# Kernel tuning notes

Hardware: AMD Instinct MI355X
Metric: run time of the kernel (lower is better)

Reference implementation:

```python
import jax, jax.numpy as jnp
import numpy as np

D_VOCAB, D_MODEL, N_CTX, D_MLP, D_HEAD, N_HEADS, N_LAYERS = 32000, 1024, 2048, 4096, 64, 16, 4
BATCH, SEQ = 2, 2048


def setup_inputs() -> dict:
    key = jax.random.key(0)
    ks = jax.random.split(key, 12)
    sd = 1.0 / np.sqrt(D_MODEL)
    inp = {
        'tokens': jax.random.randint(ks[0], (BATCH, SEQ), 0, D_VOCAB),
        'W_E': jax.random.normal(ks[1], (D_MODEL, D_VOCAB), jnp.float32) * sd,
        'W_pos': jax.random.normal(ks[2], (N_CTX, D_MODEL), jnp.float32) * sd,
        'W_K': jax.random.normal(ks[3], (N_LAYERS, N_HEADS, D_HEAD, D_MODEL), jnp.float32) * sd,
        'W_Q': jax.random.normal(ks[4], (N_LAYERS, N_HEADS, D_HEAD, D_MODEL), jnp.float32) * sd,
        'W_V': jax.random.normal(ks[5], (N_LAYERS, N_HEADS, D_HEAD, D_MODEL), jnp.float32) * sd,
        'W_O': jax.random.normal(ks[6], (N_LAYERS, D_MODEL, D_HEAD * N_HEADS), jnp.float32) * sd,
        'W_in': jax.random.normal(ks[7], (N_LAYERS, D_MLP, D_MODEL), jnp.float32) * sd,
        'b_in': jnp.zeros((N_LAYERS, D_MLP), jnp.float32),
        'W_out': jax.random.normal(ks[8], (N_LAYERS, D_MODEL, D_MLP), jnp.float32) * sd,
        'b_out': jnp.zeros((N_LAYERS, D_MODEL), jnp.float32),
        'W_U': jax.random.normal(ks[9], (D_MODEL, D_VOCAB), jnp.float32) / np.sqrt(D_VOCAB),
    }
    return inp


def reference(tokens, W_E, W_pos, W_K, W_Q, W_V, W_O, W_in, b_in, W_out, b_out, W_U):
    P = tokens.shape[-1]
    # Embed: einsum('dbp->bpd', W_E[:, x])  ==  W_E.T[tokens]
    x = W_E.T[tokens]                      # [b, p, d]
    x = x + W_pos[:P]                      # PosEmbed
    causal = jnp.tril(jnp.ones((P, P), dtype=bool))  # mask[q, p]: p <= q
    scale = 1.0 / np.sqrt(D_HEAD)
    for l in range(N_LAYERS):
        # --- Attention ---
        k = jnp.einsum('ihd,bpd->biph', W_K[l], x)
        q = jnp.einsum('ihd,bpd->biph', W_Q[l], x)
        v = jnp.einsum('ihd,bpd->biph', W_V[l], x)
        scores = jnp.einsum('biph,biqh->biqp', k, q)
        # tril(scores) - 1e10*(1-mask)  ==  where(mask, scores, -1e10)
        masked = jnp.where(causal, scores, jnp.float32(-1e10))
        attn = jax.nn.softmax(masked * scale, axis=-1)   # softmax over keys p
        z = jnp.einsum('biph,biqp->biqh', v, attn)       # [b, i, q, h]
        z_flat = jnp.transpose(z, (0, 2, 1, 3)).reshape(z.shape[0], P, -1)  # b q (i h)
        attn_out = jnp.einsum('df,bqf->bqd', W_O[l], z_flat)
        x = x + attn_out
        # --- MLP (ReLU) ---
        pre = jnp.einsum('md,bpd->bpm', W_in[l], x) + b_in[l]
        post = jax.nn.relu(pre)
        x = x + jnp.einsum('dm,bpm->bpd', W_out[l], post) + b_out[l]
    return x @ W_U                          # logits [b, p, d_vocab]
```

## Files before the change

### kernel.cpp

```cpp
#include <hip/hip_runtime.h>
#include <hip/hip_bf16.h>
#include <math.h>

#define DV   32000
#define DM   1024
#define DMLP 4096
#define DH   64
#define NH   16
#define NL   4
#define BATCH 2
#define S    2048
#define MTOK (BATCH*S)

typedef __bf16 bf16_t;
typedef bf16_t bf16x8 __attribute__((ext_vector_type(8)));
typedef float  f32x4  __attribute__((ext_vector_type(4)));

#define AS1 __attribute__((address_space(1)))
#define AS3 __attribute__((address_space(3)))

__device__ __forceinline__ void gload16(const bf16_t* g, bf16_t* l) {
    __builtin_amdgcn_global_load_lds((const AS1 void*)g, (AS3 void*)l, 16, 0, 0);
}

__device__ __forceinline__ unsigned short bfbits(float v) {
    union { bf16_t b; unsigned short u; } c; c.b = (bf16_t)v; return c.u;
}
__device__ __forceinline__ float b2f(unsigned short u) {
    union { float f; unsigned v; } c; c.v = ((unsigned)u) << 16; return c.f;
}

template<int MODE, bool BIAS, bool RELU>
__global__ __launch_bounds__(512, 1)
void gemm256(const bf16_t* __restrict__ A, const bf16_t* __restrict__ Bm,
             char* __restrict__ Out, int ldc,
             const float* __restrict__ bias, int K)
{
    const int mb = blockIdx.x, nb = blockIdx.y;

    __shared__ alignas(16) bf16_t lds[2][2][2][128*64];

    const int tid  = threadIdx.x;
    const int wave = tid >> 6, lane = tid & 63;
    const int wm = wave >> 2, wn = wave & 3;
    const int l16 = lane & 15, lh = lane >> 4;

    const bf16_t* Abase = A  + (long)(mb*256)*K;
    const bf16_t* Bbase = Bm + (long)(nb*256)*K;

    const int c0 = tid,       r0 = c0 >> 3, lc0 = (c0 & 7) ^ (r0 & 7);
    const int c1 = 512 + tid, r1 = c1 >> 3, lc1 = (c1 & 7) ^ (r1 & 7);

    auto stage = [&](int buf, int mat, int half, int k0) {
        const bf16_t* src = (mat ? Bbase : Abase) + (long)(half*128)*K + k0;
        bf16_t* dst = &lds[buf][mat][half][0];
        gload16(&src[(long)r0*K + lc0*8], dst + c0*8);
        gload16(&src[(long)r1*K + lc1*8], dst + c1*8);
    };

    f32x4 acc[8][4];
#pragma unroll
    for (int i=0;i<8;i++)
#pragma unroll
        for (int j=0;j<4;j++) { f32x4 zv={0.f,0.f,0.f,0.f}; acc[i][j]=zv; }

    const int NT = K >> 6;
    stage(0,0,0,0); stage(0,0,1,0); stage(0,1,0,0); stage(0,1,1,0);

    int cur = 0;
    for (int kt = 0; kt < NT; ++kt) {
        const int nxt = cur ^ 1;
        const int k1 = (kt+1) << 6;
        const bool more = (kt+1 < NT);

        if (more) {
            stage(nxt,0,0,k1);
            asm volatile("s_waitcnt vmcnt(2)" ::: "memory");
        } else {
            asm volatile("s_waitcnt vmcnt(0)" ::: "memory");
        }
        asm volatile("s_barrier" ::: "memory");

        bf16x8 af[4][2], bfr[4][2];
#pragma unroll
        for (int i=0;i<4;i++) {
            int ra = i*16 + l16;
#pragma unroll
            for (int kk=0;kk<2;kk++)
                af[i][kk] = *(const bf16x8*)&lds[cur][0][wm][ra*64 + (((kk*4+lh)^(ra&7))*8)];
        }
#pragma unroll
        for (int j=0;j<2;j++) {
            int rb = (wn&1)*64 + j*16 + l16;
#pragma unroll
            for (int kk=0;kk<2;kk++)
                bfr[j][kk] = *(const bf16x8*)&lds[cur][1][wn>>1][rb*64 + (((kk*4+lh)^(rb&7))*8)];
        }
        __builtin_amdgcn_s_setprio(1);
#pragma unroll
        for (int kk=0;kk<2;kk++)
#pragma unroll
            for (int i=0;i<4;i++)
#pragma unroll
                for (int j=0;j<2;j++)
                    acc[i][j] = __builtin_amdgcn_mfma_f32_16x16x32_bf16(af[i][kk], bfr[j][kk], acc[i][j], 0,0,0);
        __builtin_amdgcn_s_setprio(0);

        if (more) stage(nxt,0,1,k1);
#pragma unroll
        for (int j=2;j<4;j++) {
            int rb = (wn&1)*64 + j*16 + l16;
#pragma unroll
            for (int kk=0;kk<2;kk++)
                bfr[j][kk] = *(const bf16x8*)&lds[cur][1][wn>>1][rb*64 + (((kk*4+lh)^(rb&7))*8)];
        }
        __builtin_amdgcn_s_setprio(1);
#pragma unroll
        for (int kk=0;kk<2;kk++)
#pragma unroll
            for (int i=0;i<4;i++)
#pragma unroll
                for (int j=2;j<4;j++)
                    acc[i][j] = __builtin_amdgcn_mfma_f32_16x16x32_bf16(af[i][kk], bfr[j][kk], acc[i][j], 0,0,0);
        __builtin_amdgcn_s_setprio(0);

        if (more) stage(nxt,1,0,k1);
#pragma unroll
        for (int i=0;i<4;i++) {
            int ra = (i+4)*16 + l16;
#pragma unroll
            for (int kk=0;kk<2;kk++)
                af[i][kk] = *(const bf16x8*)&lds[cur][0][wm][ra*64 + (((kk*4+lh)^(ra&7))*8)];
        }
        __builtin_amdgcn_s_setprio(1);
#pragma unroll
        for (int kk=0;kk<2;kk++)
#pragma unroll
            for (int i=0;i<4;i++)
#pragma unroll
                for (int j=0;j<2;j++)
                    acc[i+4][j] = __builtin_amdgcn_mfma_f32_16x16x32_bf16(af[i][kk], bfr[j][kk], acc[i+4][j], 0,0,0);
        __builtin_amdgcn_s_setprio(0);

        if (more) stage(nxt,1,1,k1);
        __builtin_amdgcn_s_setprio(1);
#pragma unroll
        for (int kk=0;kk<2;kk++)
#pragma unroll
            for (int i=0;i<4;i++)
#pragma unroll
                for (int j=2;j<4;j++)
                    acc[i+4][j] = __builtin_amdgcn_mfma_f32_16x16x32_bf16(af[i][kk], bfr[j][kk], acc[i+4][j], 0,0,0);
        __builtin_amdgcn_s_setprio(0);

        asm volatile("s_barrier" ::: "memory");
        cur = nxt;
    }

    if constexpr (MODE == 1) {
        float* lsl = reinterpret_cast<float*>(&lds[0][0][0][0]) + wave*(32*68);
        const int lrow = lane >> 4;
        const int lcq  = lane & 15;
#pragma unroll
        for (int ch=0; ch<4; ++ch) {
#pragma unroll
            for (int il=0; il<2; ++il)
#pragma unroll
                for (int j=0;j<4;j++)
#pragma unroll
                    for (int r=0;r<4;r++)
                        lsl[(il*16 + lh*4 + r)*68 + j*16 + l16] = acc[ch*2+il][j][r];
#pragma unroll
            for (int u=0; u<8; ++u) {
                int rl = u*4 + lrow;
                f32x4 v = *(const f32x4*)&lsl[rl*68 + lcq*4];
                long row = mb*256 + wm*128 + ch*32 + rl;
                long col = nb*256 + wn*64 + lcq*4;
                __builtin_nontemporal_store(v, (f32x4*)&((float*)Out)[row*ldc + col]);
            }
        }
    } else {
#pragma unroll
        for (int i=0;i<8;i++) {
            int row0 = mb*256 + wm*128 + i*16 + lh*4;
#pragma unroll
            for (int j=0;j<4;j++) {
                int col = nb*256 + wn*64 + j*16 + l16;
                float bv = BIAS ? bias[col] : 0.0f;
#pragma unroll
                for (int r=0;r<4;r++) {
                    int row = row0 + r;
                    float v = acc[i][j][r] + bv;
                    if (RELU) v = v > 0.f ? v : 0.f;
                    ((bf16_t*)Out)[(long)row*ldc + col] = (bf16_t)v;
                }
            }
        }
    }
}

template<int BM, int BN, int MODE, bool BIAS, bool RELU>
__global__ __launch_bounds__(256)
void gemm_tn(const bf16_t* __restrict__ A, long sA,
             const bf16_t* __restrict__ Bm, long sB,
             char* __restrict__ Out, long sC, int ldc,
             const float* __restrict__ bias,
             float* __restrict__ resid, bf16_t* __restrict__ residb,
             int K)
{
    constexpr int BK = 64;
    constexpr int WM = BM/2, WN = BN/2;
    constexpr int FM = WM/16, FN = WN/16;
    constexpr int APASS = (BM*BK)/(256*8);
    constexpr int BPASS = (BN*BK)/(256*8);

    const int mb = blockIdx.x, nb = blockIdx.y;

    __shared__ alignas(16) bf16_t As[BM*BK];
    __shared__ alignas(16) bf16_t Bs[BN*BK];

    const int tid  = threadIdx.x;
    const int wave = tid >> 6, lane = tid & 63;
    const int wm = wave >> 1, wn = wave & 1;
    const int l16 = lane & 15, lh = lane >> 4;
    const long z = blockIdx.z;

    const bf16_t* Ab = A  + z*sA + (long)mb*BM*K;
    const bf16_t* Bb = Bm + z*sB + (long)nb*BN*K;

    f32x4 acc[FM][FN];
#pragma unroll
    for (int i=0;i<FM;i++)
#pragma unroll
        for (int j=0;j<FN;j++) { f32x4 zv = {0.f,0.f,0.f,0.f}; acc[i][j] = zv; }

    for (int k0 = 0; k0 < K; k0 += BK) {
        __syncthreads();
#pragma unroll
        for (int u=0; u<APASS; ++u) {
            int c = u*256 + tid;
            int row = c >> 3, lc = (c & 7) ^ (row & 7);
            gload16(&Ab[(long)row*K + k0 + lc*8], &As[c*8]);
        }
#pragma unroll
        for (int u=0; u<BPASS; ++u) {
            int c = u*256 + tid;
            int row = c >> 3, lc = (c & 7) ^ (row & 7);
            gload16(&Bb[(long)row*K + k0 + lc*8], &Bs[c*8]);
        }
        __syncthreads();

        bf16x8 af[FM][2], bfr[FN][2];
#pragma unroll
        for (int kk=0;kk<2;kk++) {
#pragma unroll
            for (int i=0;i<FM;i++) {
                int row = wm*WM + i*16 + l16;
                int pw = (kk*4 + lh) ^ (row & 7);
                af[i][kk] = *(const bf16x8*)&As[row*BK + pw*8];
            }
#pragma unroll
            for (int j=0;j<FN;j++) {
                int row = wn*WN + j*16 + l16;
                int pw = (kk*4 + lh) ^ (row & 7);
                bfr[j][kk] = *(const bf16x8*)&Bs[row*BK + pw*8];
            }
        }
#pragma unroll
        for (int kk=0;kk<2;kk++)
#pragma unroll
            for (int i=0;i<FM;i++)
#pragma unroll
                for (int j=0;j<FN;j++)
                    acc[i][j] = __builtin_amdgcn_mfma_f32_16x16x32_bf16(af[i][kk], bfr[j][kk], acc[i][j], 0,0,0);
    }

#pragma unroll
    for (int i=0;i<FM;i++) {
        int row0 = mb*BM + wm*WM + i*16 + lh*4;
#pragma unroll
        for (int j=0;j<FN;j++) {
            int col = nb*BN + wn*WN + j*16 + l16;
            float bv = BIAS ? bias[col] : 0.0f;
#pragma unroll
            for (int r=0;r<4;r++) {
                int row = row0 + r;
                float v = acc[i][j][r] + bv;
                if (RELU) v = v > 0.f ? v : 0.f;
                if constexpr (MODE == 0) {
                    long off = z*sC + (long)row*ldc + col;
                    ((bf16_t*)Out)[off] = (bf16_t)v;
                } else if constexpr (MODE == 1) {
                    long off = z*sC + (long)row*ldc + col;
                    ((float*)Out)[off] = v;
                } else {
                    long o2 = (long)row*ldc + col;
                    float nv = resid[o2] + v;
                    resid[o2]  = nv;
                    residb[o2] = (bf16_t)nv;
                }
            }
        }
    }
}

__global__ __launch_bounds__(256)
void flash_attn(const bf16_t* __restrict__ qkvf,
                const bf16_t* __restrict__ vtg,
                bf16_t* __restrict__ zf)
{
    const int qt = blockIdx.x;
    const int bh = blockIdx.y;
    const int b  = bh >> 4, hd = bh & 15;

    __shared__ alignas(16) bf16_t Kl[64*64];
    __shared__ alignas(16) bf16_t Vtl[64*64];
    __shared__ alignas(16) bf16_t Pl[4*32*64];

    const int tid = threadIdx.x;
    const int wave = tid >> 6, lane = tid & 63;
    const int l16 = lane & 15, lh = lane >> 4;
    const int wq_lo = qt*128 + wave*32;
    bf16_t* Pw = Pl + wave*32*64;

    bf16x8 qr[2][2];
#pragma unroll
    for (int qf=0; qf<2; qf++) {
        int qg = wq_lo + qf*16 + l16;
#pragma unroll
        for (int dhh=0; dhh<2; dhh++)
            qr[qf][dhh] = *(const bf16x8*)&qkvf[((long)b*S + qg)*3072 + hd*64 + dhh*32 + lh*8];
    }

    f32x4 o[4][2];
#pragma unroll
    for (int d=0; d<4; d++)
#pragma unroll
        for (int qf=0; qf<2; qf++) { f32x4 zv={0.f,0.f,0.f,0.f}; o[d][qf]=zv; }
    float mrun[2] = {-1e30f, -1e30f};
    float lrun[2] = {0.f, 0.f};

    const int nt = 2*(qt+1);
    const float C = 0.125f;

    for (int t = 0; t < nt; ++t) {
        const int kv0 = t*64;
        __syncthreads();
#pragma unroll
        for (int u=0; u<2; ++u) {
            int c = u*256 + tid;
            int row = c >> 3, lc = (c & 7) ^ (row & 7);
            gload16(&qkvf[((long)b*S + kv0 + row)*3072 + 1024 + hd*64 + lc*8], &Kl[c*8]);
        }
#pragma unroll
        for (int u=0; u<2; ++u) {
            int c = u*256 + tid;
            int row = c >> 3, lc = (c & 7) ^ (row & 7);
            gload16(&vtg[((long)bh*DH + row)*S + kv0 + lc*8], &Vtl[c*8]);
        }
        __syncthreads();

        f32x4 s[4][2];
#pragma unroll
        for (int f=0; f<4; f++)
#pragma unroll
            for (int qf=0; qf<2; qf++) { f32x4 zv={0.f,0.f,0.f,0.f}; s[f][qf]=zv; }
        __builtin_amdgcn_s_setprio(1);
#pragma unroll
        for (int f=0; f<4; f++) {
            int krow = f*16 + l16;
#pragma unroll
            for (int dhh=0; dhh<2; dhh++) {
                bf16x8 kfr = *(const bf16x8*)&Kl[krow*64 + (((dhh*4+lh) ^ (krow&7))*8)];
#pragma unroll
                for (int qf=0; qf<2; qf++)
                    s[f][qf] = __builtin_amdgcn_mfma_f32_16x16x32_bf16(kfr, qr[qf][dhh], s[f][qf], 0,0,0);
            }
        }
        __builtin_amdgcn_s_setprio(0);

        const bool needmask = (kv0 + 64 > wq_lo);

#pragma unroll
        for (int qf=0; qf<2; qf++) {
            int qg = wq_lo + qf*16 + l16;
            float pmax = -1e30f;
#pragma unroll
            for (int f=0; f<4; f++)
#pragma unroll
                for (int r=0; r<4; r++) {
                    float sv = s[f][qf][r];
                    if (needmask && (kv0 + f*16 + lh*4 + r > qg)) { sv = -1e30f; s[f][qf][r] = sv; }
                    pmax = fmaxf(pmax, sv);
                }
            pmax = fmaxf(pmax, __shfl_xor(pmax, 16));
            pmax = fmaxf(pmax, __shfl_xor(pmax, 32));
            float mnew = fmaxf(mrun[qf], pmax);
            float corr = __expf((mrun[qf] - mnew)*C);
            mrun[qf] = mnew;
            lrun[qf] *= corr;
#pragma unroll
            for (int d=0; d<4; d++) o[d][qf] *= corr;
            float lsum = 0.f;
            int qloc = qf*16 + l16;
#pragma unroll
            for (int f=0; f<4; f++) {
                ushort4 pk;
                float p0 = __expf((s[f][qf][0]-mnew)*C);
                float p1 = __expf((s[f][qf][1]-mnew)*C);
                float p2 = __expf((s[f][qf][2]-mnew)*C);
                float p3 = __expf((s[f][qf][3]-mnew)*C);
                lsum += (p0+p1) + (p2+p3);
                pk.x = bfbits(p0); pk.y = bfbits(p1); pk.z = bfbits(p2); pk.w = bfbits(p3);
                int phys = (f*2 + (lh>>1)) ^ (qloc & 7);
                *(ushort4*)&Pw[qloc*64 + phys*8 + (lh&1)*4] = pk;
            }
            lrun[qf] += lsum;
        }

#pragma unroll
        for (int kh=0; kh<2; kh++) {
            bf16x8 pb[2];
#pragma unroll
            for (int qf=0; qf<2; qf++) {
                int qloc = qf*16 + l16;
                pb[qf] = *(const bf16x8*)&Pw[qloc*64 + (((kh*4+lh) ^ (qloc&7))*8)];
            }
            __builtin_amdgcn_s_setprio(1);
#pragma unroll
            for (int d=0; d<4; d++) {
                int vrow = d*16 + l16;
                bf16x8 va = *(const bf16x8*)&Vtl[vrow*64 + (((kh*4+lh) ^ (vrow&7))*8)];
#pragma unroll
                for (int qf=0; qf<2; qf++)
                    o[d][qf] = __builtin_amdgcn_mfma_f32_16x16x32_bf16(va, pb[qf], o[d][qf], 0,0,0);
            }
            __builtin_amdgcn_s_setprio(0);
        }
    }

#pragma unroll
    for (int qf=0; qf<2; qf++) {
        float lt = lrun[qf];
        lt += __shfl_xor(lt, 16);
        lt += __shfl_xor(lt, 32);
        float inv = 1.0f / lt;
        int qg = wq_lo + qf*16 + l16;
#pragma unroll
        for (int d=0; d<4; d++) {
            ushort4 ov;
            ov.x = bfbits(o[d][qf][0]*inv);
            ov.y = bfbits(o[d][qf][1]*inv);
            ov.z = bfbits(o[d][qf][2]*inv);
            ov.w = bfbits(o[d][qf][3]*inv);
            *(ushort4*)&zf[((long)b*S + qg)*DM + hd*64 + d*16 + lh*4] = ov;
        }
    }
}

__global__ __launch_bounds__(256) void k_conv_qkv(
    const float* __restrict__ Wq, const float* __restrict__ Wk,
    const float* __restrict__ Wv, bf16_t* __restrict__ out)
{
    long idx = (long)blockIdx.x*256 + threadIdx.x;
    long l = idx / (3072L*DM);
    long r = idx % (3072L*DM);
    int row = (int)(r / DM), d = (int)(r % DM);
    int sel = row >> 10, rr = row & 1023;
    const float* src = sel==0 ? Wq : (sel==1 ? Wk : Wv);
    out[idx] = (bf16_t)src[(l*1024 + rr)*(long)DM + d];
}

__global__ __launch_bounds__(256) void k_conv(const float* __restrict__ src,
                                              bf16_t* __restrict__ dst, long n)
{
    long i = ((long)blockIdx.x*256 + threadIdx.x)*4;
    if (i >= n) return;
    float4 v = *(const float4*)&src[i];
    dst[i+0]=(bf16_t)v.x; dst[i+1]=(bf16_t)v.y; dst[i+2]=(bf16_t)v.z; dst[i+3]=(bf16_t)v.w;
}

__global__ __launch_bounds__(256) void k_trans(const float* __restrict__ W,
                                               bf16_t* __restrict__ out, int NC)
{
    __shared__ float tile[32][33];
    int n0 = blockIdx.x*32, k0 = blockIdx.y*32;
    int tx = threadIdx.x & 31, ty = threadIdx.x >> 5;
#pragma unroll
    for (int u=0;u<4;u++)
        tile[ty+u*8][tx] = W[(long)(k0+ty+u*8)*NC + n0+tx];
    __syncthreads();
#pragma unroll
    for (int u=0;u<4;u++)
        out[(long)(n0+ty+u*8)*DM + k0+tx] = (bf16_t)tile[tx][ty+u*8];
}

__global__ __launch_bounds__(256) void k_embed(const int* __restrict__ tok,
    const bf16_t* __restrict__ WEt, const float* __restrict__ Wpos,
    float* __restrict__ xf, bf16_t* __restrict__ xb)
{
    int bp = blockIdx.x;
    int p  = bp & (S-1);
    int t  = tok[bp];
    int d  = threadIdx.x*4;
    ushort4 e = *(const ushort4*)&WEt[(long)t*DM + d];
    float4  w = *(const float4*)&Wpos[(long)p*DM + d];
    float4 v;
    v.x = b2f(e.x)+w.x; v.y = b2f(e.y)+w.y; v.z = b2f(e.z)+w.z; v.w = b2f(e.w)+w.w;
    *(float4*)&xf[(long)bp*DM + d] = v;
    ushort4 o;
    o.x = bfbits(v.x); o.y = bfbits(v.y); o.z = bfbits(v.z); o.w = bfbits(v.w);
    *(ushort4*)&xb[(long)bp*DM + d] = o;
}

__global__ __launch_bounds__(256) void k_permv(const bf16_t* __restrict__ qkv,
    bf16_t* __restrict__ vt)
{
    __shared__ bf16_t tile[64][66];
    const int p0 = blockIdx.x*64;
    const int bh = blockIdx.y;
    const int b  = bh >> 4, hd = bh & 15;
    const int tx = threadIdx.x & 63, ty = threadIdx.x >> 6;
#pragma unroll
    for (int u=0;u<16;u++) {
        int r = u*4 + ty;
        tile[r][tx] = qkv[((long)b*S + p0 + r)*3072 + 2048 + hd*64 + tx];
    }
    __syncthreads();
#pragma unroll
    for (int u=0;u<16;u++) {
        int hh = u*4 + ty;
        vt[(((long)bh)*DH + hh)*S + p0 + tx] = tile[tx][hh];
    }
}

extern "C" void kernel_launch(void* const* d_in, const int* in_sizes, int n_in,
                              void* d_out, int out_size, void* d_ws, size_t ws_size,
                              hipStream_t stream)
{
    const int*   tokens = (const int*)d_in[0];
    const float* W_E    = (const float*)d_in[1];
    const float* W_pos  = (const float*)d_in[2];
    const float* W_K    = (const float*)d_in[3];
    const float* W_Q    = (const float*)d_in[4];
    const float* W_V    = (const float*)d_in[5];
    const float* W_O    = (const float*)d_in[6];
    const float* W_in   = (const float*)d_in[7];
    const float* b_in   = (const float*)d_in[8];
    const float* W_out  = (const float*)d_in[9];
    const float* b_out  = (const float*)d_in[10];
    const float* W_U    = (const float*)d_in[11];
    float* out = (float*)d_out;

    char* ws = (char*)d_ws;
    long off = 0;
    auto alloc = [&](long bytes)->char* {
        char* p = ws + off; off += (bytes + 255) & ~255L; return p;
    };
    bf16_t* wqkv = (bf16_t*)alloc((long)NL*3072*DM*2);
    bf16_t* wo   = (bf16_t*)alloc((long)NL*DM*DM*2);
    bf16_t* win  = (bf16_t*)alloc((long)NL*DMLP*DM*2);
    bf16_t* wout = (bf16_t*)alloc((long)NL*DM*DMLP*2);
    bf16_t* wut  = (bf16_t*)alloc((long)DV*DM*2);
    bf16_t* wet  = (bf16_t*)alloc((long)DV*DM*2);
    float*  xf   = (float*)alloc((long)MTOK*DM*4);
    bf16_t* xb   = (bf16_t*)alloc((long)MTOK*DM*2);
    bf16_t* qkvf = (bf16_t*)alloc((long)MTOK*3072*2);
    bf16_t* vt   = (bf16_t*)alloc((long)BATCH*NH*S*DH*2);
    bf16_t* zf   = (bf16_t*)alloc((long)MTOK*DM*2);
    bf16_t* post = (bf16_t*)alloc((long)MTOK*DMLP*2);

    k_conv_qkv<<<(int)(((long)NL*3072*DM)/256), 256, 0, stream>>>(W_Q, W_K, W_V, wqkv);
    k_conv<<<(int)(((long)NL*DM*DM)/1024),   256, 0, stream>>>(W_O,   wo,   (long)NL*DM*DM);
    k_conv<<<(int)(((long)NL*DMLP*DM)/1024), 256, 0, stream>>>(W_in,  win,  (long)NL*DMLP*DM);
    k_conv<<<(int)(((long)NL*DM*DMLP)/1024), 256, 0, stream>>>(W_out, wout, (long)NL*DM*DMLP);
    k_trans<<<dim3(DV/32, DM/32), 256, 0, stream>>>(W_U, wut, DV);
    k_trans<<<dim3(DV/32, DM/32), 256, 0, stream>>>(W_E, wet, DV);

    k_embed<<<MTOK, 256, 0, stream>>>(tokens, wet, W_pos, xf, xb);

    for (int l = 0; l < NL; ++l) {
        gemm256<0,false,false><<<dim3(MTOK/256, 3072/256), 512, 0, stream>>>(
            xb, wqkv + (long)l*3072*DM, (char*)qkvf, 3072, nullptr, DM);
        k_permv<<<dim3(S/64, BATCH*NH), 256, 0, stream>>>(qkvf, vt);

        flash_attn<<<dim3(S/128, BATCH*NH), 256, 0, stream>>>(qkvf, vt, zf);

        gemm_tn<128,128,2,false,false><<<dim3(MTOK/128, DM/128, 1), 256, 0, stream>>>(
            zf, 0L, wo + (long)l*DM*DM, 0L, nullptr, 0L, DM,
            nullptr, xf, xb, DM);
        gemm256<0,true,true><<<dim3(MTOK/256, DMLP/256), 512, 0, stream>>>(
            xb, win + (long)l*DMLP*DM, (char*)post, DMLP,
            b_in + (long)l*DMLP, DM);
        gemm_tn<128,128,2,true,false><<<dim3(MTOK/128, DM/128, 1), 256, 0, stream>>>(
            post, 0L, wout + (long)l*DM*DMLP, 0L, nullptr, 0L, DM,
            b_out + (long)l*DM, xf, xb, DMLP);
    }

    gemm256<1,false,false><<<dim3(MTOK/256, DV/256), 512, 0, stream>>>(
        xb, wut, (char*)out, DV, nullptr, DM);
}
```

Measured before the change: 1.651 ms.

## Add double-buffered 128x128 GEMM kernel and vectorize weight conversion

Introduces a 128x128-tile GEMM with double-buffered LDS staging, split B loads interleaved with MFMA and two blocks per CU. It replaces the single-buffered gemm_tn for the output-projection and MLP-down residual GEMMs, and replaces the 256-tile kernel for the QKV and unembedding GEMMs. The weight conversion kernels now write four bf16 values per store. The smaller tiles give more blocks to fill the CUs on narrow GEMMs but lower operand reuse on the large unembedding GEMM.

```diff
diff --git a/kernel.cpp b/kernel.cpp
--- a/kernel.cpp
+++ b/kernel.cpp
@@ -31,6 +31,156 @@
 }
 
 template<int MODE, bool BIAS, bool RELU>
+__global__ __launch_bounds__(256, 2)
+void gemm128d(const bf16_t* __restrict__ A, const bf16_t* __restrict__ Bm,
+              char* __restrict__ Out, int ldc,
+              const float* __restrict__ bias,
+              float* __restrict__ resid, bf16_t* __restrict__ residb,
+              int K)
+{
+    const int mb = blockIdx.x, nb = blockIdx.y;
+
+    __shared__ alignas(16) bf16_t lds[2][2][128*64];
+
+    const int tid  = threadIdx.x;
+    const int wave = tid >> 6, lane = tid & 63;
+    const int wm = wave >> 1, wn = wave & 1;
+    const int l16 = lane & 15, lh = lane >> 4;
+
+    const bf16_t* Abase = A  + (long)(mb*128)*K;
+    const bf16_t* Bbase = Bm + (long)(nb*128)*K;
+
+    auto stage = [&](int buf, int mat, int k0) {
+        const bf16_t* src = (mat ? Bbase : Abase) + k0;
+        bf16_t* dst = &lds[buf][mat][0];
+#pragma unroll
+        for (int u=0; u<4; ++u) {
+            int c = u*256 + tid;
+            int row = c >> 3, lc = (c & 7) ^ (row & 7);
+            gload16(&src[(long)row*K + lc*8], dst + c*8);
+        }
+    };
+
+    f32x4 acc[4][4];
+#pragma unroll
+    for (int i=0;i<4;i++)
+#pragma unroll
+        for (int j=0;j<4;j++) { f32x4 zv={0.f,0.f,0.f,0.f}; acc[i][j]=zv; }
+
+    const int NT = K >> 6;
+    stage(0,0,0); stage(0,1,0);
+
+    int cur = 0;
+    for (int kt = 0; kt < NT; ++kt) {
+        const int nxt = cur ^ 1;
+        const int k1 = (kt+1) << 6;
+        const bool more = (kt+1 < NT);
+
+        if (more) {
+            stage(nxt,0,k1);
+            asm volatile("s_waitcnt vmcnt(4)" ::: "memory");
+        } else {
+            asm volatile("s_waitcnt vmcnt(0)" ::: "memory");
+        }
+        asm volatile("s_barrier" ::: "memory");
+
+        bf16x8 af[4][2], bfr[4][2];
+#pragma unroll
+        for (int i=0;i<4;i++) {
+            int ra = wm*64 + i*16 + l16;
+#pragma unroll
+            for (int kk=0;kk<2;kk++)
+                af[i][kk] = *(const bf16x8*)&lds[cur][0][ra*64 + (((kk*4+lh)^(ra&7))*8)];
+        }
+#pragma unroll
+        for (int j=0;j<2;j++) {
+            int rb = wn*64 + j*16 + l16;
+#pragma unroll
+            for (int kk=0;kk<2;kk++)
+                bfr[j][kk] = *(const bf16x8*)&lds[cur][1][rb*64 + (((kk*4+lh)^(rb&7))*8)];
+        }
+        __builtin_amdgcn_s_setprio(1);
+#pragma unroll
+        for (int kk=0;kk<2;kk++)
+#pragma unroll
+            for (int i=0;i<4;i++)
+#pragma unroll
+                for (int j=0;j<2;j++)
+                    acc[i][j] = __builtin_amdgcn_mfma_f32_16x16x32_bf16(af[i][kk], bfr[j][kk], acc[i][j], 0,0,0);
+        __builtin_amdgcn_s_setprio(0);
+
+        if (more) stage(nxt,1,k1);
+#pragma unroll
+        for (int j=2;j<4;j++) {
+            int rb = wn*64 + j*16 + l16;
+#pragma unroll
+            for (int kk=0;kk<2;kk++)
+                bfr[j][kk] = *(const bf16x8*)&lds[cur][1][rb*64 + (((kk*4+lh)^(rb&7))*8)];
+        }
+        __builtin_amdgcn_s_setprio(1);
+#pragma unroll
+        for (int kk=0;kk<2;kk++)
+#pragma unroll
+            for (int i=0;i<4;i++)
+#pragma unroll
+                for (int j=2;j<4;j++)
+                    acc[i][j] = __builtin_amdgcn_mfma_f32_16x16x32_bf16(af[i][kk], bfr[j][kk], acc[i][j], 0,0,0);
+        __builtin_amdgcn_s_setprio(0);
+
+        asm volatile("s_barrier" ::: "memory");
+        cur = nxt;
+    }
+
+    if constexpr (MODE == 1) {
+        float* lsl = reinterpret_cast<float*>(&lds[0][0][0]) + wave*(32*68);
+        const int lrow = lane >> 4;
+        const int lcq  = lane & 15;
+#pragma unroll
+        for (int ch=0; ch<2; ++ch) {
+#pragma unroll
+            for (int il=0; il<2; ++il)
+#pragma unroll
+                for (int j=0;j<4;j++)
+#pragma unroll
+                    for (int r=0;r<4;r++)
+                        lsl[(il*16 + lh*4 + r)*68 + j*16 + l16] = acc[ch*2+il][j][r];
+#pragma unroll
+            for (int u=0; u<8; ++u) {
+                int rl = u*4 + lrow;
+                f32x4 v = *(const f32x4*)&lsl[rl*68 + lcq*4];
+                long row = mb*128 + wm*64 + ch*32 + rl;
+                long col = nb*128 + wn*64 + lcq*4;
+                __builtin_nontemporal_store(v, (f32x4*)&((float*)Out)[row*ldc + col]);
+            }
+        }
+    } else {
+#pragma unroll
+        for (int i=0;i<4;i++) {
+            int row0 = mb*128 + wm*64 + i*16 + lh*4;
+#pragma unroll
+            for (int j=0;j<4;j++) {
+                int col = nb*128 + wn*64 + j*16 + l16;
+                float bv = BIAS ? bias[col] : 0.0f;
+#pragma unroll
+                for (int r=0;r<4;r++) {
+                    int row = row0 + r;
+                    float v = acc[i][j][r] + bv;
+                    if (RELU) v = v > 0.f ? v : 0.f;
+                    if constexpr (MODE == 0) {
+                        ((bf16_t*)Out)[(long)row*ldc + col] = (bf16_t)v;
+                    } else {
+                        long o2 = (long)row*ldc + col;
+                        float nv = resid[o2] + v;
+                        resid[o2]  = nv;
+                        residb[o2] = (bf16_t)nv;
+                    }
+                }
+            }
+        }
+    }
+}
+
+template<int MODE, bool BIAS, bool RELU>
 __global__ __launch_bounds__(512, 1)
 void gemm256(const bf16_t* __restrict__ A, const bf16_t* __restrict__ Bm,
              char* __restrict__ Out, int ldc,
@@ -157,148 +307,19 @@
         cur = nxt;
     }
 
-    if constexpr (MODE == 1) {
-        float* lsl = reinterpret_cast<float*>(&lds[0][0][0][0]) + wave*(32*68);
-        const int lrow = lane >> 4;
-        const int lcq  = lane & 15;
-#pragma unroll
-        for (int ch=0; ch<4; ++ch) {
-#pragma unroll
-            for (int il=0; il<2; ++il)
-#pragma unroll
-                for (int j=0;j<4;j++)
-#pragma unroll
-                    for (int r=0;r<4;r++)
-                        lsl[(il*16 + lh*4 + r)*68 + j*16 + l16] = acc[ch*2+il][j][r];
-#pragma unroll
-            for (int u=0; u<8; ++u) {
-                int rl = u*4 + lrow;
-                f32x4 v = *(const f32x4*)&lsl[rl*68 + lcq*4];
-                long row = mb*256 + wm*128 + ch*32 + rl;
-                long col = nb*256 + wn*64 + lcq*4;
-                __builtin_nontemporal_store(v, (f32x4*)&((float*)Out)[row*ldc + col]);
-            }
-        }
-    } else {
-#pragma unroll
-        for (int i=0;i<8;i++) {
-            int row0 = mb*256 + wm*128 + i*16 + lh*4;
-#pragma unroll
-            for (int j=0;j<4;j++) {
-                int col = nb*256 + wn*64 + j*16 + l16;
-                float bv = BIAS ? bias[col] : 0.0f;
-#pragma unroll
-                for (int r=0;r<4;r++) {
-                    int row = row0 + r;
-                    float v = acc[i][j][r] + bv;
-                    if (RELU) v = v > 0.f ? v : 0.f;
-                    ((bf16_t*)Out)[(long)row*ldc + col] = (bf16_t)v;
-                }
-            }
-        }
-    }
-}
-
-template<int BM, int BN, int MODE, bool BIAS, bool RELU>
-__global__ __launch_bounds__(256)
-void gemm_tn(const bf16_t* __restrict__ A, long sA,
-             const bf16_t* __restrict__ Bm, long sB,
-             char* __restrict__ Out, long sC, int ldc,
-             const float* __restrict__ bias,
-             float* __restrict__ resid, bf16_t* __restrict__ residb,
-             int K)
-{
-    constexpr int BK = 64;
-    constexpr int WM = BM/2, WN = BN/2;
-    constexpr int FM = WM/16, FN = WN/16;
-    constexpr int APASS = (BM*BK)/(256*8);
-    constexpr int BPASS = (BN*BK)/(256*8);
-
-    const int mb = blockIdx.x, nb = blockIdx.y;
-
-    __shared__ alignas(16) bf16_t As[BM*BK];
-    __shared__ alignas(16) bf16_t Bs[BN*BK];
-
-    const int tid  = threadIdx.x;
-    const int wave = tid >> 6, lane = tid & 63;
-    const int wm = wave >> 1, wn = wave & 1;
-    const int l16 = lane & 15, lh = lane >> 4;
-    const long z = blockIdx.z;
-
-    const bf16_t* Ab = A  + z*sA + (long)mb*BM*K;
-    const bf16_t* Bb = Bm + z*sB + (long)nb*BN*K;
-
-    f32x4 acc[FM][FN];
-#pragma unroll
-    for (int i=0;i<FM;i++)
-#pragma unroll
-        for (int j=0;j<FN;j++) { f32x4 zv = {0.f,0.f,0.f,0.f}; acc[i][j] = zv; }
-
-    for (int k0 = 0; k0 < K; k0 += BK) {
-        __syncthreads();
-#pragma unroll
-        for (int u=0; u<APASS; ++u) {
-            int c = u*256 + tid;
-            int row = c >> 3, lc = (c & 7) ^ (row & 7);
-            gload16(&Ab[(long)row*K + k0 + lc*8], &As[c*8]);
-        }
-#pragma unroll
-        for (int u=0; u<BPASS; ++u) {
-            int c = u*256 + tid;
-            int row = c >> 3, lc = (c & 7) ^ (row & 7);
-            gload16(&Bb[(long)row*K + k0 + lc*8], &Bs[c*8]);
-        }
-        __syncthreads();
-
-        bf16x8 af[FM][2], bfr[FN][2];
-#pragma unroll
-        for (int kk=0;kk<2;kk++) {
-#pragma unroll
-            for (int i=0;i<FM;i++) {
-                int row = wm*WM + i*16 + l16;
-                int pw = (kk*4 + lh) ^ (row & 7);
-                af[i][kk] = *(const bf16x8*)&As[row*BK + pw*8];
-            }
-#pragma unroll
-            for (int j=0;j<FN;j++) {
-                int row = wn*WN + j*16 + l16;
-                int pw = (kk*4 + lh) ^ (row & 7);
-                bfr[j][kk] = *(const bf16x8*)&Bs[row*BK + pw*8];
-            }
-        }
-#pragma unroll
-        for (int kk=0;kk<2;kk++)
-#pragma unroll
-            for (int i=0;i<FM;i++)
-#pragma unroll
-                for (int j=0;j<FN;j++)
-                    acc[i][j] = __builtin_amdgcn_mfma_f32_16x16x32_bf16(af[i][kk], bfr[j][kk], acc[i][j], 0,0,0);
-    }
-
-#pragma unroll
-    for (int i=0;i<FM;i++) {
-        int row0 = mb*BM + wm*WM + i*16 + lh*4;
-#pragma unroll
-        for (int j=0;j<FN;j++) {
-            int col = nb*BN + wn*WN + j*16 + l16;
+#pragma unroll
+    for (int i=0;i<8;i++) {
+        int row0 = mb*256 + wm*128 + i*16 + lh*4;
+#pragma unroll
+        for (int j=0;j<4;j++) {
+            int col = nb*256 + wn*64 + j*16 + l16;
             float bv = BIAS ? bias[col] : 0.0f;
 #pragma unroll
             for (int r=0;r<4;r++) {
                 int row = row0 + r;
                 float v = acc[i][j][r] + bv;
                 if (RELU) v = v > 0.f ? v : 0.f;
-                if constexpr (MODE == 0) {
-                    long off = z*sC + (long)row*ldc + col;
-                    ((bf16_t*)Out)[off] = (bf16_t)v;
-                } else if constexpr (MODE == 1) {
-                    long off = z*sC + (long)row*ldc + col;
-                    ((float*)Out)[off] = v;
-                } else {
-                    long o2 = (long)row*ldc + col;
-                    float nv = resid[o2] + v;
-                    resid[o2]  = nv;
-                    residb[o2] = (bf16_t)nv;
-                }
+                ((bf16_t*)Out)[(long)row*ldc + col] = (bf16_t)v;
             }
         }
     }
@@ -462,13 +483,16 @@
     const float* __restrict__ Wq, const float* __restrict__ Wk,
     const float* __restrict__ Wv, bf16_t* __restrict__ out)
 {
-    long idx = (long)blockIdx.x*256 + threadIdx.x;
+    long idx = ((long)blockIdx.x*256 + threadIdx.x)*4;
     long l = idx / (3072L*DM);
     long r = idx % (3072L*DM);
     int row = (int)(r / DM), d = (int)(r % DM);
     int sel = row >> 10, rr = row & 1023;
     const float* src = sel==0 ? Wq : (sel==1 ? Wk : Wv);
-    out[idx] = (bf16_t)src[(l*1024 + rr)*(long)DM + d];
+    float4 v = *(const float4*)&src[(l*1024 + rr)*(long)DM + d];
+    ushort4 o;
+    o.x = bfbits(v.x); o.y = bfbits(v.y); o.z = bfbits(v.z); o.w = bfbits(v.w);
+    *(ushort4*)&out[idx] = o;
 }
 
 __global__ __launch_bounds__(256) void k_conv(const float* __restrict__ src,
@@ -477,7 +501,9 @@
     long i = ((long)blockIdx.x*256 + threadIdx.x)*4;
     if (i >= n) return;
     float4 v = *(const float4*)&src[i];
-    dst[i+0]=(bf16_t)v.x; dst[i+1]=(bf16_t)v.y; dst[i+2]=(bf16_t)v.z; dst[i+3]=(bf16_t)v.w;
+    ushort4 o;
+    o.x = bfbits(v.x); o.y = bfbits(v.y); o.z = bfbits(v.z); o.w = bfbits(v.w);
+    *(ushort4*)&dst[i] = o;
 }
 
 __global__ __launch_bounds__(256) void k_trans(const float* __restrict__ W,
@@ -570,7 +596,7 @@
     bf16_t* zf   = (bf16_t*)alloc((long)MTOK*DM*2);
     bf16_t* post = (bf16_t*)alloc((long)MTOK*DMLP*2);
 
-    k_conv_qkv<<<(int)(((long)NL*3072*DM)/256), 256, 0, stream>>>(W_Q, W_K, W_V, wqkv);
+    k_conv_qkv<<<(int)(((long)NL*3072*DM)/1024), 256, 0, stream>>>(W_Q, W_K, W_V, wqkv);
     k_conv<<<(int)(((long)NL*DM*DM)/1024),   256, 0, stream>>>(W_O,   wo,   (long)NL*DM*DM);
     k_conv<<<(int)(((long)NL*DMLP*DM)/1024), 256, 0, stream>>>(W_in,  win,  (long)NL*DMLP*DM);
     k_conv<<<(int)(((long)NL*DM*DMLP)/1024), 256, 0, stream>>>(W_out, wout, (long)NL*DM*DMLP);
@@ -580,23 +606,22 @@
     k_embed<<<MTOK, 256, 0, stream>>>(tokens, wet, W_pos, xf, xb);
 
     for (int l = 0; l < NL; ++l) {
-        gemm256<0,false,false><<<dim3(MTOK/256, 3072/256), 512, 0, stream>>>(
-            xb, wqkv + (long)l*3072*DM, (char*)qkvf, 3072, nullptr, DM);
+        gemm128d<0,false,false><<<dim3(MTOK/128, 3072/128), 256, 0, stream>>>(
+            xb, wqkv + (long)l*3072*DM, (char*)qkvf, 3072, nullptr, nullptr, nullptr, DM);
         k_permv<<<dim3(S/64, BATCH*NH), 256, 0, stream>>>(qkvf, vt);
 
         flash_attn<<<dim3(S/128, BATCH*NH), 256, 0, stream>>>(qkvf, vt, zf);
 
-        gemm_tn<128,128,2,false,false><<<dim3(MTOK/128, DM/128, 1), 256, 0, stream>>>(
-            zf, 0L, wo + (long)l*DM*DM, 0L, nullptr, 0L, DM,
-            nullptr, xf, xb, DM);
+        gemm128d<2,false,false><<<dim3(MTOK/128, DM/128), 256, 0, stream>>>(
+            zf, wo + (long)l*DM*DM, nullptr, DM, nullptr, xf, xb, DM);
         gemm256<0,true,true><<<dim3(MTOK/256, DMLP/256), 512, 0, stream>>>(
             xb, win + (long)l*DMLP*DM, (char*)post, DMLP,
             b_in + (long)l*DMLP, DM);
-        gemm_tn<128,128,2,true,false><<<dim3(MTOK/128, DM/128, 1), 256, 0, stream>>>(
-            post, 0L, wout + (long)l*DM*DMLP, 0L, nullptr, 0L, DM,
+        gemm128d<2,true,false><<<dim3(MTOK/128, DM/128), 256, 0, stream>>>(
+            post, wout + (long)l*DM*DMLP, nullptr, DM,
             b_out + (long)l*DM, xf, xb, DMLP);
     }
 
-    gemm256<1,false,false><<<dim3(MTOK/256, DV/256), 512, 0, stream>>>(
-        xb, wut, (char*)out, DV, nullptr, DM);
-}
+    gemm128d<1,false,false><<<dim3(MTOK/128, DV/128), 256, 0, stream>>>(
+        xb, wut, (char*)out, DV, nullptr, nullptr, nullptr, DM);
+}
```

After: 1.590 ms. -3.7%, faster.
